# Optimization experiments

Measured on AMD Instinct MI355X. Metric: run time of the kernel, lower is better.

The kernel has to match this reference:

```python
import jax, jax.numpy as jnp
import numpy as np

T_LATENCY = 2  # refractory latency (timesteps), from init_kwargs
FS_SCALE = 10.0  # FastSigmoid surrogate scale


@jax.custom_vjp
def fast_sigmoid_spike(u):
    return (u > 0).astype(u.dtype)

def _fs_fwd(u):
    return fast_sigmoid_spike(u), u

def _fs_bwd(u, g):
    return (g / (FS_SCALE * jnp.abs(u) + 1.0) ** 2,)

fast_sigmoid_spike.defvjp(_fs_fwd, _fs_bwd)


def setup_inputs() -> dict:
    key = jax.random.key(0)
    k1, k2, k3, k4 = jax.random.split(key, 4)
    B, N, T = 64, 1024, 512
    x = jax.random.normal(k1, (B, N, T), dtype=jnp.float32)
    beta = jax.random.uniform(k2, (N,), jnp.float32, 0.3, 0.95)   # leak
    p = jax.random.uniform(k3, (N,), jnp.float32, 0.5, 0.95)      # adaptation decay
    b = jax.random.uniform(k4, (N,), jnp.float32, 0.5, 1.5)       # adaptation strength
    return {"x": x, "beta": beta, "p": p, "b": b}


def reference(x, beta, p, b):
    # clamped effective params (matches torch @property accessors)
    beta_c = jnp.clip(beta, 0.001, 0.999)
    p_c = jnp.clip(jnp.abs(p), 0.0, 0.999)
    b_c = jnp.clip(jnp.abs(b), 0.001, 1.0)

    B, N, T = x.shape
    xt = jnp.moveaxis(x, 2, 0)  # [T, B, N]

    def step(carry, x_t):
        mem, spikes, refac, a, v_th = carry
        # spike-triggered refractory reset, then mask input during refractory window
        refac = jnp.where(spikes > 0, 0.0, refac)
        ic = jnp.where(refac < T_LATENCY, 0.0, x_t)
        refac = refac + 1.0
        # leaky integration
        new_mem = mem * beta_c + ic
        s = fast_sigmoid_spike(new_mem - v_th)
        # reset-by-subtraction-to-zero with detached spikes (detach_spike_grad=True)
        mem = new_mem * (1.0 - jax.lax.stop_gradient(s))
        # adaptive threshold
        a = p_c * a + s
        v_th = 1.0 + b_c * a
        return (mem, s, refac, a, v_th), s

    z = jnp.zeros((B, N), x.dtype)
    init = (z, z, jnp.full((B, N), float(T_LATENCY), x.dtype), z,
            jnp.ones((B, N), x.dtype))
    _, spikes_seq = jax.lax.scan(step, init, xt)  # [T, B, N]
    return jnp.moveaxis(spikes_seq, 0, 2)  # [B, N, T]
```

## Files before the change

kernel.cpp:

```cpp
#include <hip/hip_runtime.h>

#pragma clang fp contract(off)

#define ROWS    64
#define T_LEN   512
#define CHUNK   32
#define NCHUNK  (T_LEN / CHUNK)
#define STRIDE  (CHUNK + 4)
#define NV      8
#define NPARAM  1024

#define BARRIER() asm volatile("s_waitcnt lgkmcnt(0)\n\ts_barrier" ::: "memory")

__global__ __launch_bounds__(192) void snn_fwd(
    const float* __restrict__ x,
    const float* __restrict__ beta,
    const float* __restrict__ p,
    const float* __restrict__ bparam,
    float* __restrict__ out)
{
    __shared__ __align__(16) float inbuf [2][ROWS * STRIDE];
    __shared__ __align__(16) float outbuf[2][ROWS * STRIDE];

    const int tid     = threadIdx.x;
    const int wid     = tid >> 6;
    const int lane    = tid & 63;
    const int rowBase = blockIdx.x * ROWS;

    const float4* __restrict__ xv = (const float4*)x;
    float4* __restrict__ ov       = (float4*)out;

    const int t8 = lane & 7;
    const int r8 = lane >> 3;
    const int gq = (rowBase + r8) * (T_LEN / 4) + t8;
    const int lq = r8 * STRIDE + t8 * 4;

    float mem = 0.0f, refac = 2.0f, a = 0.0f, vth = 1.0f, ps = 0.0f;
    float beta_c = 0.f, p_c = 0.f, b_c = 0.f;
    const int cbase = lane * STRIDE;

    if (wid == 0) {
        const int n = (rowBase + lane) & (NPARAM - 1);
        beta_c = fminf(fmaxf(beta[n], 0.001f), 0.999f);
        p_c    = fminf(fabsf(p[n]), 0.999f);
        b_c    = fminf(fmaxf(fabsf(bparam[n]), 0.001f), 1.0f);
    }

    auto step = [&](float xt) -> float {
        refac = (ps > 0.0f) ? 0.0f : refac;
        const float ic = (refac < 2.0f) ? 0.0f : xt;
        refac += 1.0f;
        const float nm   = __fadd_rn(__fmul_rn(mem, beta_c), ic);
        const float diff = __fsub_rn(nm, vth);
        const float s    = (diff > 0.0f) ? 1.0f : 0.0f;
        mem = (diff > 0.0f) ? 0.0f : nm;
        a   = __fadd_rn(__fmul_rn(p_c, a), s);
        vth = __fadd_rn(1.0f, __fmul_rn(b_c, a));
        ps  = s;
        return s;
    };

    float4 ld[NV];

    auto loadChunk = [&](int k) {
        const int base = gq + k * (CHUNK / 4);
        #pragma unroll
        for (int it = 0; it < NV; ++it)
            ld[it] = xv[base + it * 8 * (T_LEN / 4)];
    };
    auto stage = [&](int buf) {
        #pragma unroll
        for (int it = 0; it < NV; ++it)
            *(float4*)&inbuf[buf][lq + it * 8 * STRIDE] = ld[it];
    };
    auto drain = [&](int buf, int k) {
        float4 sv[NV];
        #pragma unroll
        for (int it = 0; it < NV; ++it)
            sv[it] = *(const float4*)&outbuf[buf][lq + it * 8 * STRIDE];
        const int base = gq + k * (CHUNK / 4);
        #pragma unroll
        for (int it = 0; it < NV; ++it)
            ov[base + it * 8 * (T_LEN / 4)] = sv[it];
    };

    if (wid == 1) {
        loadChunk(0);
        stage(0);
        loadChunk(1);
    }
    BARRIER();

    #pragma unroll 1
    for (int k = 0; k < NCHUNK; ++k) {
        const int cur = k & 1;
        if (wid == 0) {
            #pragma unroll
            for (int t4 = 0; t4 < CHUNK / 4; ++t4) {
                float4 xq = *(const float4*)&inbuf[cur][cbase + t4 * 4];
                float4 sv;
                sv.x = step(xq.x);
                sv.y = step(xq.y);
                sv.z = step(xq.z);
                sv.w = step(xq.w);
                *(float4*)&outbuf[cur][cbase + t4 * 4] = sv;
            }
        } else if (wid == 1) {
            if (k + 1 < NCHUNK) stage(cur ^ 1);
            if (k + 2 < NCHUNK) loadChunk(k + 2);
        } else {
            if (k > 0) drain(cur ^ 1, k - 1);
        }
        BARRIER();
    }
    if (wid == 2) drain(1, NCHUNK - 1);
}

extern "C" void kernel_launch(void* const* d_in, const int* in_sizes, int n_in,
                              void* d_out, int out_size, void* d_ws, size_t ws_size,
                              hipStream_t stream) {
    const float* x    = (const float*)d_in[0];
    const float* beta = (const float*)d_in[1];
    const float* p    = (const float*)d_in[2];
    const float* b    = (const float*)d_in[3];
    float* out        = (float*)d_out;

    const int BN = 64 * 1024;
    snn_fwd<<<dim3(BN / ROWS), dim3(192), 0, stream>>>(x, beta, p, b, out);
}
```

Before: 253.4 us.

## Double chunk size, pad LDS stride to odd, single-buffer output with extra barrier

Raises the time chunk from 32 to 64 steps, so each block runs half as many chunk iterations and barriers per pair, and doubles the per-thread load batch. LDS row stride becomes CHUNK+1 (odd) to avoid bank conflicts, at the cost of scalar instead of vector LDS accesses. The output buffer is single-buffered: compute results are held in registers and written after a barrier, which adds a second barrier per chunk. Register pressure rises with 16 float4 loads and 64 spike values held per thread.

```diff
diff --git a/kernel.cpp b/kernel.cpp
--- a/kernel.cpp
+++ b/kernel.cpp
@@ -4,10 +4,10 @@
 
 #define ROWS    64
 #define T_LEN   512
-#define CHUNK   32
+#define CHUNK   64
 #define NCHUNK  (T_LEN / CHUNK)
-#define STRIDE  (CHUNK + 4)
-#define NV      8
+#define STRIDE  (CHUNK + 1)
+#define NV      16
 #define NPARAM  1024
 
 #define BARRIER() asm volatile("s_waitcnt lgkmcnt(0)\n\ts_barrier" ::: "memory")
@@ -19,8 +19,8 @@
     const float* __restrict__ bparam,
     float* __restrict__ out)
 {
-    __shared__ __align__(16) float inbuf [2][ROWS * STRIDE];
-    __shared__ __align__(16) float outbuf[2][ROWS * STRIDE];
+    __shared__ float inbuf[2][ROWS * STRIDE];
+    __shared__ float outbuf[ROWS * STRIDE];
 
     const int tid     = threadIdx.x;
     const int wid     = tid >> 6;
@@ -30,14 +30,14 @@
     const float4* __restrict__ xv = (const float4*)x;
     float4* __restrict__ ov       = (float4*)out;
 
-    const int t8 = lane & 7;
-    const int r8 = lane >> 3;
-    const int gq = (rowBase + r8) * (T_LEN / 4) + t8;
-    const int lq = r8 * STRIDE + t8 * 4;
+    const int t16 = lane & 15;
+    const int r4  = lane >> 4;
+    const int gq  = (rowBase + r4) * (T_LEN / 4) + t16;
+    const int lf  = r4 * STRIDE + t16 * 4;
 
     float mem = 0.0f, refac = 2.0f, a = 0.0f, vth = 1.0f, ps = 0.0f;
     float beta_c = 0.f, p_c = 0.f, b_c = 0.f;
-    const int cbase = lane * STRIDE;
+    const int cb = lane * STRIDE;
 
     if (wid == 0) {
         const int n = (rowBase + lane) & (NPARAM - 1);
@@ -63,25 +63,33 @@
     float4 ld[NV];
 
     auto loadChunk = [&](int k) {
-        const int base = gq + k * (CHUNK / 4);
+        const int base = gq + k * NV;
         #pragma unroll
         for (int it = 0; it < NV; ++it)
-            ld[it] = xv[base + it * 8 * (T_LEN / 4)];
+            ld[it] = xv[base + it * 4 * (T_LEN / 4)];
     };
     auto stage = [&](int buf) {
         #pragma unroll
-        for (int it = 0; it < NV; ++it)
-            *(float4*)&inbuf[buf][lq + it * 8 * STRIDE] = ld[it];
+        for (int it = 0; it < NV; ++it) {
+            const int o = lf + it * 4 * STRIDE;
+            inbuf[buf][o + 0] = ld[it].x;
+            inbuf[buf][o + 1] = ld[it].y;
+            inbuf[buf][o + 2] = ld[it].z;
+            inbuf[buf][o + 3] = ld[it].w;
+        }
     };
-    auto drain = [&](int buf, int k) {
-        float4 sv[NV];
+    auto drain = [&](int k) {
+        const int base = gq + k * NV;
         #pragma unroll
-        for (int it = 0; it < NV; ++it)
-            sv[it] = *(const float4*)&outbuf[buf][lq + it * 8 * STRIDE];
-        const int base = gq + k * (CHUNK / 4);
-        #pragma unroll
-        for (int it = 0; it < NV; ++it)
-            ov[base + it * 8 * (T_LEN / 4)] = sv[it];
+        for (int it = 0; it < NV; ++it) {
+            const int o = lf + it * 4 * STRIDE;
+            float4 sv;
+            sv.x = outbuf[o + 0];
+            sv.y = outbuf[o + 1];
+            sv.z = outbuf[o + 2];
+            sv.w = outbuf[o + 3];
+            ov[base + it * 4 * (T_LEN / 4)] = sv;
+        }
     };
 
     if (wid == 1) {
@@ -94,26 +102,26 @@
     #pragma unroll 1
     for (int k = 0; k < NCHUNK; ++k) {
         const int cur = k & 1;
+        float sv[CHUNK];
         if (wid == 0) {
             #pragma unroll
-            for (int t4 = 0; t4 < CHUNK / 4; ++t4) {
-                float4 xq = *(const float4*)&inbuf[cur][cbase + t4 * 4];
-                float4 sv;
-                sv.x = step(xq.x);
-                sv.y = step(xq.y);
-                sv.z = step(xq.z);
-                sv.w = step(xq.w);
-                *(float4*)&outbuf[cur][cbase + t4 * 4] = sv;
-            }
+            for (int t = 0; t < CHUNK; ++t)
+                sv[t] = step(inbuf[cur][cb + t]);
         } else if (wid == 1) {
             if (k + 1 < NCHUNK) stage(cur ^ 1);
             if (k + 2 < NCHUNK) loadChunk(k + 2);
         } else {
-            if (k > 0) drain(cur ^ 1, k - 1);
+            if (k > 0) drain(k - 1);
+        }
+        BARRIER();
+        if (wid == 0) {
+            #pragma unroll
+            for (int t = 0; t < CHUNK; ++t)
+                outbuf[cb + t] = sv[t];
         }
         BARRIER();
     }
-    if (wid == 2) drain(1, NCHUNK - 1);
+    if (wid == 2) drain(NCHUNK - 1);
 }
 
 extern "C" void kernel_launch(void* const* d_in, const int* in_sizes, int n_in,
```

New measurement: 241.4 us. -4.7%, faster.
